# Kernel optimization log

Hardware: AMD Instinct MI355X
Metric: run time of the kernel (lower is better)

The kernel has to match this reference:

```python
import jax, jax.numpy as jnp
import numpy as np

B, L, NSTATE = 8192, 256, 9


def setup_inputs() -> dict:
    key = jax.random.key(0)
    k1, k2, k3, k4 = jax.random.split(key, 4)
    inputs = jax.random.normal(k1, (B, L, NSTATE), dtype=jnp.float32)
    path = jax.random.randint(k2, (B, L), 0, NSTATE, dtype=jnp.int32)
    # learned CRF params (init'd to zeros in the module; use small random for a
    # non-degenerate reference)
    tran = jax.random.normal(k3, (NSTATE, NSTATE), dtype=jnp.float32) * 0.1
    init = jax.random.normal(k4, (NSTATE,), dtype=jnp.float32) * 0.1
    return {"inputs": inputs, "path": path, "tran": tran, "init": init}


def reference(inputs, path, tran, init):
    # inputs: [B, L, S], path: [B, L], tran: [S, S], init: [S]
    # bio=False -> mask and imask are all zeros (no-op additions).
    # --- gold path score ---
    emit = jnp.take_along_axis(inputs, path[..., None], axis=-1)[..., 0]  # [B, L]
    tran_sc = tran[path[..., :-1], path[..., 1:]]                         # [B, L-1]
    path_scores = emit.sum(-1) + init[path[..., 0]] + tran_sc.sum(-1)     # [B]

    # --- partition function via log-semiring forward recurrence ---
    alpha0 = init + inputs[..., 0, :]                                     # [B, S]

    def step(alpha, x_t):
        # alpha: [B, S] (prev state), x_t: [B, S] (emission at t)
        nxt = alpha[..., :, None] + tran + x_t[..., None, :]              # [B, S, S]
        return jax.nn.logsumexp(nxt, axis=-2), None

    xs = jnp.moveaxis(inputs[..., 1:, :], -2, 0)                          # [L-1, B, S]
    alpha, _ = jax.lax.scan(step, alpha0, xs)
    scores = jax.nn.logsumexp(alpha, axis=-1)                             # [B]
    return scores - path_scores
```

## Files before the change

kernel.cpp:

```cpp
#include <hip/hip_runtime.h>


#define B_N 8192
#define L_N 256
#define SEQ_STRIDE 2304
#define HALF 128
#define SPB 6
#define XW 54
#define XSTRIDE 55
#define NBLK 22
#define PLS 129
#define SPW 16
#define NBLOCKS (B_N / SPW)

#define LOG2E 1.44269504088896340736f
#define LN2f  0.69314718055994530942f

#define QP1 57
#define QP2 78
#define QP3 147
#define QROT(src, CTRL) \
  __int_as_float(__builtin_amdgcn_mov_dpp(__float_as_int(src), CTRL, 0xf, 0xf, 0))

#define WAITV(N) asm volatile("s_waitcnt vmcnt(" #N ")" ::: "memory")

__device__ __forceinline__ void gl_lds4(const void* g, void* l) {
  __builtin_amdgcn_global_load_lds(
      (const __attribute__((address_space(1))) void*)g,
      (__attribute__((address_space(3))) void*)l, 4, 0, 0);
}

__device__ __forceinline__ float fexp(float x) {
  return __builtin_amdgcn_exp2f(x * LOG2E);
}

__global__ __launch_bounds__(128, 1) void crf_fused(
    const float* __restrict__ xg, const int* __restrict__ path,
    const float* __restrict__ tran, const float* __restrict__ initv,
    float* __restrict__ out)
{
  __shared__ float lx[2][3][SPW * XSTRIDE];
  __shared__ int   pl[2][SPW * PLS];
  __shared__ float ltran[2][81];
  __shared__ float comb[2][SPW][11];

  const int tid  = threadIdx.x;
  const int w    = tid >> 6;
  const int lane = tid & 63;
  const int c = lane & 3;
  const int q = lane >> 2;
  const bool fwd = (w == 0);
  const int seq0 = blockIdx.x * SPW;

  for (int i = lane; i < 81; i += 64) ltran[w][i] = tran[i];

  float Erot[4][3][3];
#pragma unroll
  for (int r = 0; r < 4; ++r)
#pragma unroll
    for (int k = 0; k < 3; ++k)
#pragma unroll
      for (int i = 0; i < 3; ++i) {
        const int ig = 3 * c + i;
        const int jg = 3 * ((c + r) & 3) + k;
        float v = 0.f;
        if (ig < 9 && jg < 9)
          v = fexp(fwd ? tran[jg * 9 + ig] : tran[ig * 9 + jg]);
        Erot[r][k][i] = v;
      }

  float iv[3];
#pragma unroll
  for (int k = 0; k < 3; ++k) {
    iv[k] = (fwd && c < 3) ? initv[3 * c + k] : 0.f;
    asm volatile("" :: "v"(iv[k]));
  }

  float o[3];
  float emit = 0.f, trn = 0.f;
  int ce = 0, pcur = 0;
  if (!fwd) {
#pragma unroll
    for (int k = 0; k < 3; ++k) o[k] = (c < 3) ? 1.f : 0.f;
    pcur = path[(size_t)(seq0 + q) * L_N + 255];
  }
  asm volatile("" :: "v"(pcur));
  const int myoff = (c == 3) ? 0 : 3 * c;

  {
    const int t0 = fwd ? 0 : 127;
#pragma unroll
    for (int r = 0; r < SPW; ++r) {
      const int* g = path + (size_t)(seq0 + r) * L_N + t0 + lane;
      gl_lds4(g,      &pl[w][r * PLS]);
      gl_lds4(g + 64, &pl[w][r * PLS + 64]);
    }
  }
  if (lane < XW) {
#pragma unroll
    for (int wi = 0; wi < 2; ++wi) {
      const int fb = fwd ? wi * XW : (SEQ_STRIDE - XW * (wi + 1));
#pragma unroll
      for (int r = 0; r < SPW; ++r)
        gl_lds4(xg + (size_t)(seq0 + r) * SEQ_STRIDE + fb + lane,
                &lx[w][wi][r * XSTRIDE]);
    }
  }

#pragma unroll 1
  for (int b = 0; b < NBLK; ++b) {
    if (b + 2 < NBLK) {
      if (lane < XW) {
        const int fb = fwd ? (b + 2) * XW : (SEQ_STRIDE - XW * (b + 3));
        float* dst = &lx[w][(b + 2) % 3][0];
#pragma unroll
        for (int r = 0; r < SPW; ++r)
          gl_lds4(xg + (size_t)(seq0 + r) * SEQ_STRIDE + fb + lane,
                  dst + r * XSTRIDE);
      }
      WAITV(32);
    } else if (b + 1 < NBLK) {
      WAITV(16);
    } else {
      WAITV(0);
    }

    const float* lxq = &lx[w][b % 3][q * XSTRIDE];

    float e[SPB * 3];
#pragma unroll
    for (int tt = 0; tt < SPB; ++tt)
#pragma unroll
      for (int k = 0; k < 3; ++k)
        e[tt * 3 + k] = fexp(lxq[tt * 9 + myoff + k]);

    if (fwd) {
#pragma unroll
      for (int kk = 0; kk < SPB; ++kk) {
        const int t = b * SPB + kk;
        if (t < HALF) {
          if (t == 0) {
#pragma unroll
            for (int k = 0; k < 3; ++k)
              o[k] = (c < 3) ? fexp(iv[k] + lxq[myoff + k]) : 0.f;
            pcur = pl[w][q * PLS];
            emit = lxq[pcur];
          } else {
            float g[4][3];
#pragma unroll
            for (int k = 0; k < 3; ++k) {
              g[0][k] = o[k];
              g[1][k] = QROT(o[k], QP1);
              g[2][k] = QROT(o[k], QP2);
              g[3][k] = QROT(o[k], QP3);
            }
            if (kk == 0 && b > 0) {
              float m = g[0][0];
#pragma unroll
              for (int r = 0; r < 4; ++r)
#pragma unroll
                for (int k = 0; k < 3; ++k) m = fmaxf(m, g[r][k]);
              const int ex = (int)((__float_as_uint(m) >> 23) & 0xffu) - 126;
              ce += ex;
              const float sc = __uint_as_float((unsigned)(127 - ex) << 23);
#pragma unroll
              for (int r = 0; r < 4; ++r)
#pragma unroll
                for (int k = 0; k < 3; ++k) g[r][k] *= sc;
            }
            float out3[3];
#pragma unroll
            for (int i = 0; i < 3; ++i) {
              float a = Erot[0][0][i] * g[0][0];
#pragma unroll
              for (int r = 0; r < 4; ++r)
#pragma unroll
                for (int k = 0; k < 3; ++k)
                  if (r + k > 0) a = fmaf(Erot[r][k][i], g[r][k], a);
              out3[i] = a;
            }
            const int p = pl[w][q * PLS + t];
            emit += lxq[kk * 9 + p];
            trn  += ltran[w][pcur * 9 + p];
            pcur = p;
#pragma unroll
            for (int i = 0; i < 3; ++i) o[i] = out3[i] * e[kk * 3 + i];
          }
        }
      }
    } else {
#pragma unroll
      for (int kk = 0; kk < SPB; ++kk) {
        const int t = 255 - b * SPB - kk;
        if (t >= HALF) {
          const int tt = SPB - 1 - kk;
          float wv[3];
#pragma unroll
          for (int k = 0; k < 3; ++k) wv[k] = e[tt * 3 + k] * o[k];
          float g[4][3];
#pragma unroll
          for (int k = 0; k < 3; ++k) {
            g[0][k] = wv[k];
            g[1][k] = QROT(wv[k], QP1);
            g[2][k] = QROT(wv[k], QP2);
            g[3][k] = QROT(wv[k], QP3);
          }
          if (kk == 0 && b > 0) {
            float m = g[0][0];
#pragma unroll
            for (int r = 0; r < 4; ++r)
#pragma unroll
              for (int k = 0; k < 3; ++k) m = fmaxf(m, g[r][k]);
            const int ex = (int)((__float_as_uint(m) >> 23) & 0xffu) - 126;
            ce += ex;
            const float sc = __uint_as_float((unsigned)(127 - ex) << 23);
#pragma unroll
            for (int r = 0; r < 4; ++r)
#pragma unroll
              for (int k = 0; k < 3; ++k) g[r][k] *= sc;
          }
#pragma unroll
          for (int i = 0; i < 3; ++i) {
            float a = Erot[0][0][i] * g[0][0];
#pragma unroll
            for (int r = 0; r < 4; ++r)
#pragma unroll
              for (int k = 0; k < 3; ++k)
                if (r + k > 0) a = fmaf(Erot[r][k][i], g[r][k], a);
            o[i] = a;
          }
          emit += lxq[tt * 9 + pcur];
          const int pm = pl[w][q * PLS + (t - 1 - 127)];
          trn += ltran[w][pm * 9 + pcur];
          pcur = pm;
        }
      }
    }
  }

  if (c < 3) {
#pragma unroll
    for (int k = 0; k < 3; ++k) comb[w][q][3 * c + k] = o[k];
  } else {
    comb[w][q][9]  = (float)ce;
    comb[w][q][10] = fwd ? (emit + trn + initv[pl[w][q * PLS]])
                         : (emit + trn);
  }
  __syncthreads();

  if (tid < SPW) {
    float dot = 0.f;
#pragma unroll
    for (int i = 0; i < 9; ++i)
      dot = fmaf(comb[0][tid][i], comb[1][tid][i], dot);
    const float score =
        (__builtin_amdgcn_logf(dot) + comb[0][tid][9] + comb[1][tid][9]) * LN2f;
    out[seq0 + tid] = score - (comb[0][tid][10] + comb[1][tid][10]);
  }
}

extern "C" void kernel_launch(void* const* d_in, const int* in_sizes, int n_in,
                              void* d_out, int out_size, void* d_ws, size_t ws_size,
                              hipStream_t stream) {
  (void)in_sizes; (void)n_in; (void)out_size; (void)d_ws; (void)ws_size;
  const float* xg    = (const float*)d_in[0];
  const int*   path  = (const int*)d_in[1];
  const float* tran  = (const float*)d_in[2];
  const float* initv = (const float*)d_in[3];
  float* out = (float*)d_out;

  crf_fused<<<NBLOCKS, 128, 0, stream>>>(xg, path, tran, initv, out);
}
```

Baseline: 145.5 us.

## Batch path-score LDS lookups per block and shrink emission prefetch to double buffer

The gold-path emission and transition lookups are hoisted out of the serial recurrence. They are gathered for all six steps of each block up front and accumulated after the recurrence, so the dependent LDS reads no longer interleave with the DPP/FMA chain. The emission prefetch drops from three buffers with two blocks in flight to two buffers with one block in flight, waiting on all loads each iteration. This reduces LDS use and simplifies the waits, but exposes more global-load latency because prefetch distance is now only one block.

```diff
diff --git a/kernel.cpp b/kernel.cpp
--- a/kernel.cpp
+++ b/kernel.cpp
@@ -39,7 +39,7 @@
     const float* __restrict__ tran, const float* __restrict__ initv,
     float* __restrict__ out)
 {
-  __shared__ float lx[2][3][SPW * XSTRIDE];
+  __shared__ float lx[2][2][SPW * XSTRIDE];
   __shared__ int   pl[2][SPW * PLS];
   __shared__ float ltran[2][81];
   __shared__ float comb[2][SPW][11];
@@ -97,35 +97,46 @@
     }
   }
   if (lane < XW) {
-#pragma unroll
-    for (int wi = 0; wi < 2; ++wi) {
-      const int fb = fwd ? wi * XW : (SEQ_STRIDE - XW * (wi + 1));
+    const int fb = fwd ? 0 : (SEQ_STRIDE - XW);
+#pragma unroll
+    for (int r = 0; r < SPW; ++r)
+      gl_lds4(xg + (size_t)(seq0 + r) * SEQ_STRIDE + fb + lane,
+              &lx[w][0][r * XSTRIDE]);
+  }
+
+  const int*   plr = &pl[w][q * PLS];
+  const float* ltw = ltran[w];
+
+#pragma unroll 1
+  for (int b = 0; b < NBLK; ++b) {
+    WAITV(0);
+
+    if (b + 1 < NBLK && lane < XW) {
+      const int fb = fwd ? (b + 1) * XW : (SEQ_STRIDE - XW * (b + 2));
+      float* dst = &lx[w][(b + 1) & 1][0];
 #pragma unroll
       for (int r = 0; r < SPW; ++r)
         gl_lds4(xg + (size_t)(seq0 + r) * SEQ_STRIDE + fb + lane,
-                &lx[w][wi][r * XSTRIDE]);
-    }
-  }
-
-#pragma unroll 1
-  for (int b = 0; b < NBLK; ++b) {
-    if (b + 2 < NBLK) {
-      if (lane < XW) {
-        const int fb = fwd ? (b + 2) * XW : (SEQ_STRIDE - XW * (b + 3));
-        float* dst = &lx[w][(b + 2) % 3][0];
-#pragma unroll
-        for (int r = 0; r < SPW; ++r)
-          gl_lds4(xg + (size_t)(seq0 + r) * SEQ_STRIDE + fb + lane,
-                  dst + r * XSTRIDE);
-      }
-      WAITV(32);
-    } else if (b + 1 < NBLK) {
-      WAITV(16);
+                dst + r * XSTRIDE);
+    }
+
+    const float* lxq = &lx[w][b & 1][q * XSTRIDE];
+    const int tb = b * SPB;
+
+    int p[SPB];
+    if (fwd) {
+#pragma unroll
+      for (int kk = 0; kk < SPB; ++kk) {
+        int t = tb + kk; if (t > HALF - 1) t = HALF - 1;
+        p[kk] = plr[t];
+      }
     } else {
-      WAITV(0);
-    }
-
-    const float* lxq = &lx[w][b % 3][q * XSTRIDE];
+#pragma unroll
+      for (int kk = 0; kk < SPB; ++kk) {
+        int idx = 127 - tb - kk; if (idx < 0) idx = 0;
+        p[kk] = plr[idx];
+      }
+    }
 
     float e[SPB * 3];
 #pragma unroll
@@ -134,17 +145,33 @@
       for (int k = 0; k < 3; ++k)
         e[tt * 3 + k] = fexp(lxq[tt * 9 + myoff + k]);
 
+    float em[SPB], tr[SPB];
     if (fwd) {
 #pragma unroll
       for (int kk = 0; kk < SPB; ++kk) {
-        const int t = b * SPB + kk;
+        em[kk] = lxq[kk * 9 + p[kk]];
+        const int pp = kk ? p[kk - 1] : pcur;
+        tr[kk] = ltw[pp * 9 + p[kk]];
+      }
+    } else {
+#pragma unroll
+      for (int kk = 0; kk < SPB; ++kk) {
+        const int pc = kk ? p[kk - 1] : pcur;
+        em[kk] = lxq[(SPB - 1 - kk) * 9 + pc];
+        tr[kk] = ltw[p[kk] * 9 + pc];
+      }
+    }
+    pcur = p[SPB - 1];
+
+    if (fwd) {
+#pragma unroll
+      for (int kk = 0; kk < SPB; ++kk) {
+        const int t = tb + kk;
         if (t < HALF) {
           if (t == 0) {
 #pragma unroll
             for (int k = 0; k < 3; ++k)
               o[k] = (c < 3) ? fexp(iv[k] + lxq[myoff + k]) : 0.f;
-            pcur = pl[w][q * PLS];
-            emit = lxq[pcur];
           } else {
             float g[4][3];
 #pragma unroll
@@ -179,10 +206,6 @@
                   if (r + k > 0) a = fmaf(Erot[r][k][i], g[r][k], a);
               out3[i] = a;
             }
-            const int p = pl[w][q * PLS + t];
-            emit += lxq[kk * 9 + p];
-            trn  += ltran[w][pcur * 9 + p];
-            pcur = p;
 #pragma unroll
             for (int i = 0; i < 3; ++i) o[i] = out3[i] * e[kk * 3 + i];
           }
@@ -191,7 +214,7 @@
     } else {
 #pragma unroll
       for (int kk = 0; kk < SPB; ++kk) {
-        const int t = 255 - b * SPB - kk;
+        const int t = 255 - tb - kk;
         if (t >= HALF) {
           const int tt = SPB - 1 - kk;
           float wv[3];
@@ -229,11 +252,23 @@
                 if (r + k > 0) a = fmaf(Erot[r][k][i], g[r][k], a);
             o[i] = a;
           }
-          emit += lxq[tt * 9 + pcur];
-          const int pm = pl[w][q * PLS + (t - 1 - 127)];
-          trn += ltran[w][pm * 9 + pcur];
-          pcur = pm;
         }
+      }
+    }
+
+    if (fwd) {
+#pragma unroll
+      for (int kk = 0; kk < SPB; ++kk) {
+        const int t = tb + kk;
+        if (t < HALF) {
+          emit += em[kk];
+          if (kk > 0 || b > 0) trn += tr[kk];
+        }
+      }
+    } else {
+#pragma unroll
+      for (int kk = 0; kk < SPB; ++kk) {
+        if (255 - tb - kk >= HALF) { emit += em[kk]; trn += tr[kk]; }
       }
     }
   }
@@ -243,7 +278,7 @@
     for (int k = 0; k < 3; ++k) comb[w][q][3 * c + k] = o[k];
   } else {
     comb[w][q][9]  = (float)ce;
-    comb[w][q][10] = fwd ? (emit + trn + initv[pl[w][q * PLS]])
+    comb[w][q][10] = fwd ? (emit + trn + initv[plr[0]])
                          : (emit + trn);
   }
   __syncthreads();
```

New measurement: 145.5 us. About the same (-0.0%).
